# Performance work log

Measured on AMD Instinct MI355X. Metric: run time of the kernel, lower is better.

The kernel has to match this reference:

```python
import jax, jax.numpy as jnp
import numpy as np

N_NODES = 50000
N_EDGES = 1600000
HIDDEN = 128
HEADS = 8
HEAD_DIM = HIDDEN // HEADS


def setup_inputs() -> dict:
    key = jax.random.key(0)
    ks = jax.random.split(key, 6)
    s = 1.0 / np.sqrt(HIDDEN)
    return {
        "h":   jax.random.normal(ks[0], (N_NODES, HIDDEN), dtype=jnp.float32),
        "W_Q": jax.random.normal(ks[1], (HIDDEN, HIDDEN), dtype=jnp.float32) * s,
        "b_Q": jnp.zeros((HIDDEN,), jnp.float32),
        "W_K": jax.random.normal(ks[2], (HIDDEN, HIDDEN), dtype=jnp.float32) * s,
        "b_K": jnp.zeros((HIDDEN,), jnp.float32),
        "W_V": jax.random.normal(ks[3], (HIDDEN, HIDDEN), dtype=jnp.float32) * s,
        "b_V": jnp.zeros((HIDDEN,), jnp.float32),
        "src": jax.random.randint(ks[4], (N_EDGES,), 0, N_NODES, dtype=jnp.int32),
        "dst": jax.random.randint(ks[5], (N_EDGES,), 0, N_NODES, dtype=jnp.int32),
    }


def _gcn_conv(h, W, b, src, dst, norm_out, norm_in):
    # DGL GraphConv, norm='both', in_feats == out_feats -> aggregate then matmul
    feat = h * norm_out[:, None]                                   # [N, H]
    agg = jax.ops.segment_sum(feat[src], dst, num_segments=N_NODES)  # [N, H]
    agg = agg * norm_in[:, None]
    return agg @ W + b


def reference(h, W_Q, b_Q, W_K, b_K, W_V, b_V, src, dst):
    ones = jnp.ones((N_EDGES,), jnp.float32)
    deg_out = jnp.clip(jax.ops.segment_sum(ones, src, num_segments=N_NODES), 1.0)
    deg_in = jnp.clip(jax.ops.segment_sum(ones, dst, num_segments=N_NODES), 1.0)
    norm_out = jax.lax.rsqrt(deg_out)
    norm_in = jax.lax.rsqrt(deg_in)

    Q = jax.nn.relu(_gcn_conv(h, W_Q, b_Q, src, dst, norm_out, norm_in))
    K = jax.nn.relu(_gcn_conv(h, W_K, b_K, src, dst, norm_out, norm_in))
    V = jax.nn.relu(_gcn_conv(h, W_V, b_V, src, dst, norm_out, norm_in))

    Qh = Q.reshape(N_NODES, HEADS, HEAD_DIM)
    Kh = K.reshape(N_NODES, HEADS, HEAD_DIM)
    Vh = V.reshape(N_NODES, HEADS, HEAD_DIM)

    # per-edge attention: score_e = <K[src], Q[dst]> per head, exp-clamped
    scale = np.sqrt(HEAD_DIM).astype(np.float32)
    score = jnp.sum(Kh[src] * Qh[dst], axis=-1)                    # [E, heads]
    score = jnp.exp(jnp.clip(score / scale, -10.0, 10.0))

    wV = jax.ops.segment_sum(Vh[src] * score[:, :, None], dst, num_segments=N_NODES)  # [N, heads, d]
    z = jax.ops.segment_sum(score, dst, num_segments=N_NODES)     # [N, heads]
    return wV / (z[:, :, None] + 1e-6)
```

## Files before the change

kernel.cpp:

```cpp
#include <hip/hip_runtime.h>

#define N_NODES 50000
#define N_EDGES 1600000
#define CAP 64
#define OVF_CAP 8192

#define O_CNTO   0
#define O_CNTI   50000
#define O_OVFN   100000
#define O_OVF    100002
#define O_BUCKET 120000
#define O_HB     3320000
#define O_AGGB   6520000
#define O_WT     9720000
#define O_QB     9750000
#define O_KV     12950000

typedef unsigned int uint;
typedef __attribute__((ext_vector_type(8))) short short8;
typedef __attribute__((ext_vector_type(4))) float floatx4;

union U16 { uint4 u; short8 s; };

__device__ __forceinline__ uint f2bf2(float a, float b) {
    uint ua = __float_as_uint(a); ua = (ua + 0x7fffu + ((ua >> 16) & 1u)) >> 16;
    uint ub = __float_as_uint(b); ub = (ub + 0x7fffu + ((ub >> 16) & 1u)) >> 16;
    return ua | (ub << 16);
}
__device__ __forceinline__ float bflo(uint u) { return __uint_as_float(u << 16); }
__device__ __forceinline__ float bfhi(uint u) { return __uint_as_float(u & 0xffff0000u); }

__global__ __launch_bounds__(256) void k_build(const int* __restrict__ src,
                                               const int* __restrict__ dst,
                                               int* cnt_out, int* cnt_in,
                                               int* __restrict__ bucket,
                                               int* ovf_n, int2* __restrict__ ovf) {
    int e = blockIdx.x * 256 + threadIdx.x;
    if (e < N_EDGES) {
        int s = src[e], d = dst[e];
        atomicAdd(&cnt_out[s], 1);
        int pos = atomicAdd(&cnt_in[d], 1);
        if (pos < CAP) {
            bucket[(d << 6) + pos] = s;
        } else {
            int o = atomicAdd(ovf_n, 1);
            if (o < OVF_CAP) ovf[o] = make_int2(d, s);
        }
    }
}

__global__ __launch_bounds__(256) void k_wt(const float* __restrict__ WQ,
                                            const float* __restrict__ WK,
                                            const float* __restrict__ WV,
                                            uint* __restrict__ wt) {
    int idx = blockIdx.x * 256 + threadIdx.x;
    if (idx < 3 * 8192) {
        int y = idx >> 13;
        int rem = idx & 8191;
        int k2 = rem >> 7;
        int n  = rem & 127;
        const float* W = (y == 0) ? WQ : (y == 1) ? WK : WV;
        float a = W[(2 * k2) * 128 + n];
        float b = W[(2 * k2 + 1) * 128 + n];
        wt[(y << 13) + (n << 6) + k2] = f2bf2(a, b);
    }
}

__global__ __launch_bounds__(256) void k_hb(const float* __restrict__ h,
                                            const int* __restrict__ cnt_out,
                                            uint* __restrict__ hb) {
    int idx = blockIdx.x * 256 + threadIdx.x;
    if (idx < N_NODES * 64) {
        int n = idx >> 6;
        float no = rsqrtf(fmaxf((float)cnt_out[n], 1.0f));
        float2 hv = *(const float2*)(h + ((size_t)idx << 1));
        hb[idx] = f2bf2(hv.x * no, hv.y * no);
    }
}

__global__ __launch_bounds__(256) void k_agg(
    const int* __restrict__ cnt_in, const int* __restrict__ bucket,
    const int* __restrict__ ovf_n, const int2* __restrict__ ovf,
    const uint* __restrict__ hb, uint* __restrict__ aggb)
{
    int n = blockIdx.x * 4 + (threadIdx.x >> 6);
    int lane = threadIdx.x & 63;
    int cnt = cnt_in[n];
    int m = min(cnt, CAP);
    const int* b = bucket + ((size_t)n << 6);
    float ax = 0.f, ay = 0.f;
    int i = 0;
    for (; i + 8 <= m; i += 8) {
        int s[8]; uint u[8];
        #pragma unroll
        for (int j = 0; j < 8; ++j) s[j] = b[i + j];
        #pragma unroll
        for (int j = 0; j < 8; ++j) u[j] = hb[((size_t)s[j] << 6) + lane];
        #pragma unroll
        for (int j = 0; j < 8; ++j) { ax += bflo(u[j]); ay += bfhi(u[j]); }
    }
    for (; i < m; ++i) {
        int s = b[i];
        uint u = hb[((size_t)s << 6) + lane];
        ax += bflo(u);
        ay += bfhi(u);
    }
    if (cnt > CAP) {
        int on = min(*ovf_n, OVF_CAP);
        for (int j = 0; j < on; ++j) {
            int2 p = ovf[j];
            if (p.x == n) {
                uint u = hb[((size_t)p.y << 6) + lane];
                ax += bflo(u);
                ay += bfhi(u);
            }
        }
    }
    float ni = rsqrtf(fmaxf((float)cnt, 1.0f));
    aggb[((size_t)n << 6) + lane] = f2bf2(ax * ni, ay * ni);
}

__global__ __launch_bounds__(256) void k_qkv(
    const uint* __restrict__ aggb, const uint* __restrict__ wt,
    const float* __restrict__ bQ, const float* __restrict__ bK,
    const float* __restrict__ bV,
    uint* __restrict__ qb, uint* __restrict__ kv)
{
    const int y = blockIdx.y;
    const int row0 = blockIdx.x * 128;
    const float* bias = (y == 0) ? bQ : (y == 1) ? bK : bV;

    __shared__ uint sA[128 * 68];

    const int t = threadIdx.x;
    for (int idx = t; idx < 128 * 16; idx += 256) {
        int r = idx >> 4, c4 = (idx & 15) << 2;
        int row = row0 + r;
        uint4 v = make_uint4(0u, 0u, 0u, 0u);
        if (row < N_NODES) v = *(const uint4*)(aggb + ((size_t)row << 6) + c4);
        *(uint4*)(&sA[r * 68 + c4]) = v;
    }
    __syncthreads();

    const int wave = t >> 6;
    const int lane = t & 63;
    const int mrow = lane & 15;
    const int kq   = lane >> 4;
    const int mbase = wave * 32;
    const uint* wty = wt + (y << 13);

    floatx4 acc[2][8];
    for (int a = 0; a < 2; ++a)
        for (int b = 0; b < 8; ++b)
            acc[a][b] = (floatx4){0.f, 0.f, 0.f, 0.f};

    for (int kc = 0; kc < 128; kc += 32) {
        int koff = (kc >> 1) + (kq << 2);
        short8 afr[2], bfr[8];
        for (int mt = 0; mt < 2; ++mt) {
            U16 u; u.u = *(const uint4*)(&sA[(mbase + mt * 16 + mrow) * 68 + koff]);
            afr[mt] = u.s;
        }
        for (int nt = 0; nt < 8; ++nt) {
            U16 u; u.u = *(const uint4*)(wty + ((nt * 16 + mrow) << 6) + koff);
            bfr[nt] = u.s;
        }
        for (int mt = 0; mt < 2; ++mt)
            for (int nt = 0; nt < 8; ++nt)
                acc[mt][nt] = __builtin_amdgcn_mfma_f32_16x16x32_bf16(
                    afr[mt], bfr[nt], acc[mt][nt], 0, 0, 0);
    }

    if (y == 0) {
        for (int mt = 0; mt < 2; ++mt) {
            int rbase = row0 + mbase + mt * 16 + kq * 4;
            for (int nt = 0; nt < 8; ++nt) {
                int c = nt * 16 + mrow;
                float bv = bias[c];
                for (int r = 0; r < 4; ++r) {
                    float v = fmaxf(acc[mt][nt][r] + bv, 0.f);
                    float pv = __shfl_xor(v, 1);
                    int row = rbase + r;
                    if (((lane & 1) == 0) && row < N_NODES)
                        qb[((size_t)row << 6) + (c >> 1)] = f2bf2(v, pv);
                }
            }
        }
    } else {
        const int vo = (y == 2) ? 1 : 0;
        for (int mt = 0; mt < 2; ++mt) {
            int rbase = row0 + mbase + mt * 16 + kq * 4;
            for (int nt = 0; nt < 8; ++nt) {
                int c = nt * 16 + mrow;
                float bv = bias[c];
                for (int r = 0; r < 4; ++r) {
                    float v = fmaxf(acc[mt][nt][r] + bv, 0.f);
                    float pv = __shfl_xor(v, 1);
                    int row = rbase + r;
                    if (((lane & 1) == 0) && row < N_NODES)
                        kv[((size_t)row << 7) + c + vo] = f2bf2(v, pv);
                }
            }
        }
    }
}

__device__ __forceinline__ void attn_step(uint2 kvp, float qx, float qy,
                                          float& ax, float& ay, float& zacc) {
    float p = bflo(kvp.x) * qx + bfhi(kvp.x) * qy;
    p += __shfl_xor(p, 1);
    p += __shfl_xor(p, 2);
    p += __shfl_xor(p, 4);
    float sc = __expf(fminf(fmaxf(p * 0.25f, -10.f), 10.f));
    ax += bflo(kvp.y) * sc;
    ay += bfhi(kvp.y) * sc;
    zacc += sc;
}

__global__ __launch_bounds__(256) void k_attn(
    const int* __restrict__ cnt_in, const int* __restrict__ bucket,
    const int* __restrict__ ovf_n, const int2* __restrict__ ovf,
    const uint* __restrict__ qb, const uint* __restrict__ kv,
    float* __restrict__ out)
{
    int n = blockIdx.x * 4 + (threadIdx.x >> 6);
    int lane = threadIdx.x & 63;
    int cnt = cnt_in[n];
    int m = min(cnt, CAP);
    const int* b = bucket + ((size_t)n << 6);

    uint qu = qb[((size_t)n << 6) + lane];
    float qx = bflo(qu), qy = bfhi(qu);
    float ax = 0.f, ay = 0.f, zacc = 0.f;

    int i = 0;
    for (; i + 8 <= m; i += 8) {
        int s[8]; uint2 p[8];
        #pragma unroll
        for (int j = 0; j < 8; ++j) s[j] = b[i + j];
        #pragma unroll
        for (int j = 0; j < 8; ++j)
            p[j] = *(const uint2*)(kv + ((size_t)s[j] << 7) + (lane << 1));
        #pragma unroll
        for (int j = 0; j < 8; ++j)
            attn_step(p[j], qx, qy, ax, ay, zacc);
    }
    for (; i < m; ++i) {
        int s = b[i];
        uint2 p = *(const uint2*)(kv + ((size_t)s << 7) + (lane << 1));
        attn_step(p, qx, qy, ax, ay, zacc);
    }
    if (cnt > CAP) {
        int on = min(*ovf_n, OVF_CAP);
        for (int j = 0; j < on; ++j) {
            int2 pr = ovf[j];
            if (pr.x == n) {
                uint2 p = *(const uint2*)(kv + ((size_t)pr.y << 7) + (lane << 1));
                attn_step(p, qx, qy, ax, ay, zacc);
            }
        }
    }

    float inv = 1.0f / (zacc + 1e-6f);
    float2 o; o.x = ax * inv; o.y = ay * inv;
    *(float2*)(out + ((size_t)n << 7) + (lane << 1)) = o;
}

extern "C" void kernel_launch(void* const* d_in, const int* in_sizes, int n_in,
                              void* d_out, int out_size, void* d_ws, size_t ws_size,
                              hipStream_t stream) {
    const float* h   = (const float*)d_in[0];
    const float* WQ  = (const float*)d_in[1];
    const float* bQ  = (const float*)d_in[2];
    const float* WK  = (const float*)d_in[3];
    const float* bK  = (const float*)d_in[4];
    const float* WV  = (const float*)d_in[5];
    const float* bV  = (const float*)d_in[6];
    const int*   src = (const int*)d_in[7];
    const int*   dst = (const int*)d_in[8];
    float* out = (float*)d_out;
    float* ws  = (float*)d_ws;
    int*   wsi = (int*)d_ws;

    int*   cnt_out = wsi + O_CNTO;
    int*   cnt_in  = wsi + O_CNTI;
    int*   ovf_n   = wsi + O_OVFN;
    int2*  ovf     = (int2*)(wsi + O_OVF);
    int*   bucket  = wsi + O_BUCKET;
    uint*  hb      = (uint*)(ws + O_HB);
    uint*  aggb    = (uint*)(ws + O_AGGB);
    uint*  wt      = (uint*)(ws + O_WT);
    uint*  qb      = (uint*)(ws + O_QB);
    uint*  kv      = (uint*)(ws + O_KV);

    hipMemsetAsync(wsi, 0, (2 * N_NODES + 2) * sizeof(int), stream);

    k_wt<<<(3 * 8192 + 255) / 256, 256, 0, stream>>>(WQ, WK, WV, wt);
    k_build<<<N_EDGES / 256, 256, 0, stream>>>(src, dst, cnt_out, cnt_in,
                                               bucket, ovf_n, ovf);
    k_hb<<<(N_NODES * 64 + 255) / 256, 256, 0, stream>>>(h, cnt_out, hb);

    k_agg<<<N_NODES / 4, 256, 0, stream>>>(cnt_in, bucket, ovf_n, ovf, hb, aggb);

    dim3 g_qkv((N_NODES + 127) / 128, 3);
    k_qkv<<<g_qkv, 256, 0, stream>>>(aggb, wt, bQ, bK, bV, qb, kv);

    k_attn<<<N_NODES / 4, 256, 0, stream>>>(cnt_in, bucket, ovf_n, ovf,
                                            qb, kv, out);
}
```

Measured before the change: 463.1 us.

## Build CSR buckets via two-pass binned partition with shared-memory atomics

```diff
diff --git a/kernel.cpp b/kernel.cpp
--- a/kernel.cpp
+++ b/kernel.cpp
@@ -5,16 +5,24 @@
 #define CAP 64
 #define OVF_CAP 8192
 
+#define BIN_SHIFT 7
+#define BIN_NODES 128
+#define NBINS 391
+#define BIN_CAP 5120
+#define EPB 4096
+
 #define O_CNTO   0
 #define O_CNTI   50000
 #define O_OVFN   100000
 #define O_OVF    100002
+#define O_BINC   116400
 #define O_BUCKET 120000
 #define O_HB     3320000
 #define O_AGGB   6520000
 #define O_WT     9720000
 #define O_QB     9750000
 #define O_KV     12950000
+#define O_PAIRS  3320000
 
 typedef unsigned int uint;
 typedef __attribute__((ext_vector_type(8))) short short8;
@@ -30,22 +38,78 @@
 __device__ __forceinline__ float bflo(uint u) { return __uint_as_float(u << 16); }
 __device__ __forceinline__ float bfhi(uint u) { return __uint_as_float(u & 0xffff0000u); }
 
-__global__ __launch_bounds__(256) void k_build(const int* __restrict__ src,
-                                               const int* __restrict__ dst,
-                                               int* cnt_out, int* cnt_in,
-                                               int* __restrict__ bucket,
-                                               int* ovf_n, int2* __restrict__ ovf) {
-    int e = blockIdx.x * 256 + threadIdx.x;
-    if (e < N_EDGES) {
-        int s = src[e], d = dst[e];
-        atomicAdd(&cnt_out[s], 1);
-        int pos = atomicAdd(&cnt_in[d], 1);
+__global__ __launch_bounds__(256) void k_part(const int* __restrict__ src,
+                                              const int* __restrict__ dst,
+                                              int* cnt_out,
+                                              int* bin_cnt,
+                                              int2* __restrict__ pairs) {
+    __shared__ int hist[NBINS];
+    __shared__ int base[NBINS];
+    const int t = threadIdx.x;
+    const int e0 = blockIdx.x * EPB;
+
+    for (int b = t; b < NBINS; b += 256) hist[b] = 0;
+    __syncthreads();
+
+    #pragma unroll
+    for (int i = 0; i < EPB / 256; ++i) {
+        int e = e0 + i * 256 + t;
+        if (e < N_EDGES) {
+            int d = dst[e];
+            atomicAdd(&hist[d >> BIN_SHIFT], 1);
+            atomicAdd(&cnt_out[src[e]], 1);
+        }
+    }
+    __syncthreads();
+
+    for (int b = t; b < NBINS; b += 256) {
+        base[b] = atomicAdd(&bin_cnt[b], hist[b]);
+        hist[b] = 0;
+    }
+    __syncthreads();
+
+    #pragma unroll
+    for (int i = 0; i < EPB / 256; ++i) {
+        int e = e0 + i * 256 + t;
+        if (e < N_EDGES) {
+            int d = dst[e], s = src[e];
+            int bin = d >> BIN_SHIFT;
+            int idx = base[bin] + atomicAdd(&hist[bin], 1);
+            if (idx < BIN_CAP)
+                pairs[(size_t)bin * BIN_CAP + idx] = make_int2(d, s);
+        }
+    }
+}
+
+__global__ __launch_bounds__(256) void k_bins(const int* __restrict__ bin_cnt,
+                                              const int2* __restrict__ pairs,
+                                              int* __restrict__ cnt_in,
+                                              int* __restrict__ bucket,
+                                              int* ovf_n, int2* __restrict__ ovf) {
+    __shared__ int lcnt[BIN_NODES];
+    const int b = blockIdx.x;
+    const int t = threadIdx.x;
+    for (int i = t; i < BIN_NODES; i += 256) lcnt[i] = 0;
+    __syncthreads();
+
+    const int nb = min(bin_cnt[b], BIN_CAP);
+    const int2* pp = pairs + (size_t)b * BIN_CAP;
+    for (int i = t; i < nb; i += 256) {
+        int2 p = pp[i];
+        int pos = atomicAdd(&lcnt[p.x & (BIN_NODES - 1)], 1);
         if (pos < CAP) {
-            bucket[(d << 6) + pos] = s;
+            bucket[((size_t)p.x << 6) + pos] = p.y;
         } else {
             int o = atomicAdd(ovf_n, 1);
-            if (o < OVF_CAP) ovf[o] = make_int2(d, s);
-        }
+            if (o < OVF_CAP) ovf[o] = p;
+        }
+    }
+    __syncthreads();
+
+    const int node0 = b << BIN_SHIFT;
+    for (int i = t; i < BIN_NODES; i += 256) {
+        int n = node0 + i;
+        if (n < N_NODES) cnt_in[n] = lcnt[i];
     }
 }
 
@@ -286,18 +350,23 @@
     int*   cnt_in  = wsi + O_CNTI;
     int*   ovf_n   = wsi + O_OVFN;
     int2*  ovf     = (int2*)(wsi + O_OVF);
+    int*   bin_cnt = wsi + O_BINC;
     int*   bucket  = wsi + O_BUCKET;
+    int2*  pairs   = (int2*)(wsi + O_PAIRS);
     uint*  hb      = (uint*)(ws + O_HB);
     uint*  aggb    = (uint*)(ws + O_AGGB);
     uint*  wt      = (uint*)(ws + O_WT);
     uint*  qb      = (uint*)(ws + O_QB);
     uint*  kv      = (uint*)(ws + O_KV);
 
-    hipMemsetAsync(wsi, 0, (2 * N_NODES + 2) * sizeof(int), stream);
+    hipMemsetAsync(wsi, 0, (O_BINC + NBINS) * sizeof(int), stream);
 
     k_wt<<<(3 * 8192 + 255) / 256, 256, 0, stream>>>(WQ, WK, WV, wt);
-    k_build<<<N_EDGES / 256, 256, 0, stream>>>(src, dst, cnt_out, cnt_in,
-                                               bucket, ovf_n, ovf);
+
+    k_part<<<(N_EDGES + EPB - 1) / EPB, 256, 0, stream>>>(src, dst, cnt_out,
+                                                          bin_cnt, pairs);
+    k_bins<<<NBINS, 256, 0, stream>>>(bin_cnt, pairs, cnt_in, bucket, ovf_n, ovf);
+
     k_hb<<<(N_NODES * 64 + 255) / 256, 256, 0, stream>>>(h, cnt_out, hb);
 
     k_agg<<<N_NODES / 4, 256, 0, stream>>>(cnt_in, bucket, ovf_n, ovf, hb, aggb);
```

New measurement: 416.4 us. -10.1%, faster.
